# Performance work log

Measured on AMD Instinct MI355X. Metric: run time of the kernel, lower is better.

## Reference

```python
import jax, jax.numpy as jnp
import numpy as np

FP8_MAX = 448.0   # max finite value of float8_e4m3fn
GROUP = 128       # quant group size (both act cols and weight blocks)


def fp8_roundtrip(v):
    # Round-to-nearest onto the fp8 e4m3fn grid, back to f32.
    return v.astype(jnp.float8_e4m3fn).astype(jnp.float32)


def setup_inputs() -> dict:
    key = jax.random.key(0)
    k1, k2, k3 = jax.random.split(key, 3)
    M, H = 8192, 4096
    x = jax.random.normal(k1, (M, 2 * H), dtype=jnp.float32)
    # weight: rand -> fp8 grid (stored as f32 values lying exactly on fp8 grid)
    w_q = fp8_roundtrip(jax.random.uniform(k2, (H, H), dtype=jnp.float32))
    # per-(128,128)-block weight scales
    wscale = jax.random.uniform(k3, (H // GROUP, H // GROUP), dtype=jnp.float32)
    return {"x": x, "w_q": w_q, "wscale": wscale}


def reference(x, w_q, wscale):
    H = x.shape[-1] // 2
    # SiluAndMul: silu(gate) * up
    y = jax.nn.silu(x[:, :H]) * x[:, H:]            # [M, H]
    M = y.shape[0]
    # --- activation group quant, group shape (1, 128) ---
    g = y.reshape(M, H // GROUP, GROUP)
    amax = jnp.max(jnp.abs(g), axis=-1, keepdims=True)
    scale = jnp.maximum(amax, 1e-12) / FP8_MAX      # [M, H/128, 1]
    q = fp8_roundtrip(g / scale)                    # fp8-grid values
    y_dq = (q * scale).reshape(M, H)                # dequantized activation
    # --- weight block dequant, block shape (128, 128) ---
    nk, nn = H // GROUP, H // GROUP
    w_dq = (w_q.reshape(nk, GROUP, nn, GROUP) * wscale[:, None, :, None]).reshape(H, H)
    # block-fp8 linear: out[m, n] = sum_k y_dq[m, k] * w_dq[k, n]
    return y_dq @ w_dq
```

## Files before the change

kernel.cpp:

```cpp
#include <hip/hip_runtime.h>
#include <hip/hip_fp8.h>
#include <hip/hip_bf16.h>

#define MDIM 8192
#define HDIM 4096
#define NKT 64

typedef float f32x4 __attribute__((ext_vector_type(4)));
typedef short bf16x8 __attribute__((ext_vector_type(8)));
typedef unsigned short u16x4 __attribute__((ext_vector_type(4)));

__device__ inline void gload_lds16(const void* g, void* l) {
  __builtin_amdgcn_global_load_lds(
      (const __attribute__((address_space(1))) void*)g,
      (__attribute__((address_space(3))) void*)l, 16, 0, 0);
}

__device__ inline unsigned short f2bf(float f) {
  __hip_bfloat16 h = __float2bfloat16(f);
  return *reinterpret_cast<unsigned short*>(&h);
}

__global__ __launch_bounds__(256) void silu_quant_kernel(
    const float* __restrict__ x, unsigned short* __restrict__ yb) {
  const int m = blockIdx.x;
  const int t = threadIdx.x;
  const int g = t >> 3;
  const int i = t & 7;
  const float* xr = x + (size_t)m * (2 * HDIM);

  float v[16];
  float amax = 0.f;
#pragma unroll
  for (int j = 0; j < 4; ++j) {
    const int off = g * 128 + j * 32 + i * 4;
    f32x4 gate = *(const f32x4*)(xr + off);
    f32x4 up = *(const f32x4*)(xr + HDIM + off);
#pragma unroll
    for (int c = 0; c < 4; ++c) {
      float gg = gate[c];
      float s = gg / (1.f + expf(-gg));
      float val = s * up[c];
      v[j * 4 + c] = val;
      amax = fmaxf(amax, fabsf(val));
    }
  }
#pragma unroll
  for (int d = 1; d < 8; d <<= 1) amax = fmaxf(amax, __shfl_xor(amax, d, 64));
  const float scale = fmaxf(amax, 1e-12f) / 448.0f;

#pragma unroll
  for (int j = 0; j < 4; ++j) {
    u16x4 pk;
#pragma unroll
    for (int c = 0; c < 4; ++c) {
      __hip_fp8_e4m3 qv(v[j * 4 + c] / scale);
      pk[c] = f2bf((float)qv * scale);
    }
    *(u16x4*)(yb + (size_t)m * HDIM + g * 128 + j * 32 + i * 4) = pk;
  }
}

__global__ __launch_bounds__(256) void wconv_kernel(
    const float* __restrict__ w, const float* __restrict__ wsc,
    unsigned short* __restrict__ wt) {
  __shared__ unsigned short tile[64][66];
  const int t = threadIdx.x;
  const int n0 = (blockIdx.x & 63) * 64;
  const int k0 = (blockIdx.x >> 6) * 64;
  const float ws = wsc[(k0 >> 7) * 32 + (n0 >> 7)];
  {
    const int r = t >> 4;
    const int c4 = (t & 15) << 2;
#pragma unroll
    for (int j = 0; j < 4; ++j) {
      const int kr = r + j * 16;
      f32x4 vv = *(const f32x4*)(w + (size_t)(k0 + kr) * HDIM + n0 + c4);
#pragma unroll
      for (int c = 0; c < 4; ++c) tile[kr][c4 + c] = f2bf(vv[c] * ws);
    }
  }
  __syncthreads();
  {
    const int n = t >> 4;
    const int k4 = (t & 15) << 2;
#pragma unroll
    for (int j = 0; j < 4; ++j) {
      const int nn = n + j * 16;
      u16x4 pk;
#pragma unroll
      for (int c = 0; c < 4; ++c) pk[c] = tile[k4 + c][nn];
      *(u16x4*)(wt + (size_t)(n0 + nn) * HDIM + k0 + k4) = pk;
    }
  }
}

#define SCHED0 __builtin_amdgcn_sched_barrier(0)
#define SBAR do { SCHED0; __builtin_amdgcn_s_barrier(); SCHED0; } while (0)
#define VMW(n) asm volatile("s_waitcnt vmcnt(" #n ")" ::: "memory")
#define LGKM0 asm volatile("s_waitcnt lgkmcnt(0)" ::: "memory")
#define PRIO1 __builtin_amdgcn_s_setprio(1)
#define PRIO0 __builtin_amdgcn_s_setprio(0)

#define STAGE_UNIT(bi, kt, u) do {                                          \
    const __hip_bfloat16* gsrc;  unsigned char* ldst;                       \
    if ((u) == 0)      { gsrc = A + (size_t)(m0 + r0) * HDIM;       ldst = As[bi]; }          \
    else if ((u) == 1) { gsrc = B + (size_t)(n0 + r0) * HDIM;       ldst = Bs[bi]; }          \
    else if ((u) == 2) { gsrc = A + (size_t)(m0 + 128 + r0) * HDIM; ldst = As[bi] + 16384; }  \
    else               { gsrc = B + (size_t)(n0 + 128 + r0) * HDIM; ldst = Bs[bi] + 16384; }  \
    gsrc += (size_t)(kt) * 64 + cst * 8;                                    \
    gload_lds16(gsrc, ldst + t * 16);                                       \
    gload_lds16(gsrc + (size_t)64 * HDIM, ldst + 8192 + t * 16);            \
  } while (0)

#define RD_A(c, mh, dst) do { _Pragma("unroll") for (int mi = 0; mi < 4; ++mi) { \
    const int row = wm * 128 + (mh) * 64 + mi * 16 + lrow;                       \
    _Pragma("unroll") for (int kk = 0; kk < 2; ++kk)                             \
      dst[mi][kk] = *(const bf16x8*)(As[c] + row * 128 + (((kk * 4 + lhi) ^ rx) * 16)); \
  } } while (0)

#define RD_B(c, nh, dst) do { _Pragma("unroll") for (int ni = 0; ni < 2; ++ni) { \
    const int row = wn * 64 + (nh) * 32 + ni * 16 + lrow;                        \
    _Pragma("unroll") for (int kk = 0; kk < 2; ++kk)                             \
      dst[ni][kk] = *(const bf16x8*)(Bs[c] + row * 128 + (((kk * 4 + lhi) ^ rx) * 16)); \
  } } while (0)

#define MFMA16(AF, BF, MB, NB) do { _Pragma("unroll") for (int kk = 0; kk < 2; ++kk) \
    _Pragma("unroll") for (int mi = 0; mi < 4; ++mi)                                 \
      _Pragma("unroll") for (int ni = 0; ni < 2; ++ni)                               \
        acc[(MB) + mi][(NB) + ni] = __builtin_amdgcn_mfma_f32_16x16x32_bf16(         \
            AF[mi][kk], BF[ni][kk], acc[(MB) + mi][(NB) + ni], 0, 0, 0);             \
  } while (0)

#define ITER(j, SH123, SH0, VMSTMT) do {                                     \
    const int c_ = (j) & 1, n_ = c_ ^ 1;                                     \
                                                     \
    RD_A(c_, 0, afr0); RD_B(c_, 0, bfr0);                                    \
    if (SH123) STAGE_UNIT(n_, (j) + 1, 1);                                   \
    SCHED0;                                                                  \
    PRIO1; MFMA16(afr0, bfr0, 0, 0); PRIO0;                                  \
                                                     \
    RD_A(c_, 1, afr1);                                                       \
    if (SH123) STAGE_UNIT(n_, (j) + 1, 2);                                   \
    SCHED0;                                                                  \
    PRIO1; MFMA16(afr1, bfr0, 4, 0); PRIO0;                                  \
                                                     \
    RD_B(c_, 1, bfr1);                                                       \
    if (SH123) STAGE_UNIT(n_, (j) + 1, 3);                                   \
    SCHED0;                                                                  \
    PRIO1; MFMA16(afr1, bfr1, 4, 2); PRIO0;                                  \
    LGKM0; SBAR;                 \
                                                     \
    if (SH0) STAGE_UNIT(c_, (j) + 2, 0);                                     \
    SCHED0;                                                                  \
    PRIO1; MFMA16(afr0, bfr1, 0, 2); PRIO0;                                  \
    VMSTMT; SBAR;                                                            \
  } while (0)

__global__ __launch_bounds__(512, 1) void gemm_bf16_kernel(
    const __hip_bfloat16* __restrict__ A,
    const __hip_bfloat16* __restrict__ B,
    float* __restrict__ out) {
  __shared__ __align__(16) unsigned char As[2][32768];
  __shared__ __align__(16) unsigned char Bs[2][32768];

  const int bid = blockIdx.x;
  const int x = bid & 7, sub = bid >> 3;
  const int mtile = (x >> 1) * 8 + (sub & 7);
  const int ntile = (x & 1) * 8 + (sub >> 3);
  const int m0 = mtile * 256, n0 = ntile * 256;

  const int t = threadIdx.x;
  const int l = t & 63, wid = t >> 6;
  const int wm = wid >> 2, wn = wid & 3;
  const int lrow = l & 15, lhi = l >> 4;
  const int rx = lrow & 7;

  const int r0 = t >> 3;
  const int cst = (t & 7) ^ (r0 & 7);

  f32x4 acc[8][4];
#pragma unroll
  for (int a = 0; a < 8; ++a)
#pragma unroll
    for (int b = 0; b < 4; ++b) acc[a][b] = (f32x4){0.f, 0.f, 0.f, 0.f};
  bf16x8 afr0[4][2], afr1[4][2], bfr0[2][2], bfr1[2][2];

  STAGE_UNIT(0, 0, 0); STAGE_UNIT(0, 0, 1); STAGE_UNIT(0, 0, 2); STAGE_UNIT(0, 0, 3);
  STAGE_UNIT(1, 1, 0);
  VMW(2);
  SBAR;

  for (int j = 0; j <= NKT - 3; ++j) ITER(j, 1, 1, VMW(2));
  ITER(NKT - 2, 1, 0, VMW(0));
  ITER(NKT - 1, 0, 0, (void)0);

#pragma unroll
  for (int mi = 0; mi < 8; ++mi)
#pragma unroll
    for (int r = 0; r < 4; ++r) {
      const int grow = m0 + wm * 128 + mi * 16 + lhi * 4 + r;
      float* orow = out + (size_t)grow * HDIM + n0 + wn * 64 + lrow;
#pragma unroll
      for (int ni = 0; ni < 4; ++ni) orow[ni * 16] = acc[mi][ni][r];
    }
}

extern "C" void kernel_launch(void* const* d_in, const int* in_sizes, int n_in,
                              void* d_out, int out_size, void* d_ws, size_t ws_size,
                              hipStream_t stream) {
  const float* x = (const float*)d_in[0];
  const float* wq = (const float*)d_in[1];
  const float* wsc = (const float*)d_in[2];
  float* out = (float*)d_out;

  unsigned short* yb = (unsigned short*)d_ws;
  unsigned short* wt = yb + (size_t)MDIM * HDIM;

  silu_quant_kernel<<<MDIM, 256, 0, stream>>>(x, yb);
  wconv_kernel<<<(HDIM / 64) * (HDIM / 64), 256, 0, stream>>>(wq, wsc, wt);
  gemm_bf16_kernel<<<(MDIM / 256) * (HDIM / 256), 512, 0, stream>>>(
      (const __hip_bfloat16*)yb, (const __hip_bfloat16*)wt, out);
}
```

Before: 310.5 us.

## Simplify GEMM pipeline to single-tile prefetch with extra barriers per phase

Replaces the staggered prefetch schedule, where the A-low unit was loaded two k-tiles ahead and waits used vmcnt(2), with a plain double buffer. All four units of the next tile are issued in the first two phases, and the loop waits for vmcnt(0) at the end of each iteration. It adds a workgroup barrier around every MFMA phase, which lets the waves run in lockstep. The cost is less latency hiding, because each tile's loads must finish within one iteration, plus more barrier stalls.

```diff
diff --git a/kernel.cpp b/kernel.cpp
--- a/kernel.cpp
+++ b/kernel.cpp
@@ -97,7 +97,7 @@
 
 #define SCHED0 __builtin_amdgcn_sched_barrier(0)
 #define SBAR do { SCHED0; __builtin_amdgcn_s_barrier(); SCHED0; } while (0)
-#define VMW(n) asm volatile("s_waitcnt vmcnt(" #n ")" ::: "memory")
+#define VMW0 asm volatile("s_waitcnt vmcnt(0)" ::: "memory")
 #define LGKM0 asm volatile("s_waitcnt lgkmcnt(0)" ::: "memory")
 #define PRIO1 __builtin_amdgcn_s_setprio(1)
 #define PRIO0 __builtin_amdgcn_s_setprio(0)
@@ -132,29 +132,28 @@
             AF[mi][kk], BF[ni][kk], acc[(MB) + mi][(NB) + ni], 0, 0, 0);             \
   } while (0)
 
-#define ITER(j, SH123, SH0, VMSTMT) do {                                     \
+#define ITER(j, SH) do {                                                     \
     const int c_ = (j) & 1, n_ = c_ ^ 1;                                     \
-                                                     \
+                          \
     RD_A(c_, 0, afr0); RD_B(c_, 0, bfr0);                                    \
-    if (SH123) STAGE_UNIT(n_, (j) + 1, 1);                                   \
-    SCHED0;                                                                  \
+    if (SH) { STAGE_UNIT(n_, (j) + 1, 0); STAGE_UNIT(n_, (j) + 1, 1); }      \
+    SBAR; LGKM0; SCHED0;                                                     \
     PRIO1; MFMA16(afr0, bfr0, 0, 0); PRIO0;                                  \
-                                                     \
+    SBAR;                                                                    \
+                          \
     RD_A(c_, 1, afr1);                                                       \
-    if (SH123) STAGE_UNIT(n_, (j) + 1, 2);                                   \
-    SCHED0;                                                                  \
+    if (SH) { STAGE_UNIT(n_, (j) + 1, 2); STAGE_UNIT(n_, (j) + 1, 3); }      \
+    SBAR; LGKM0; SCHED0;                                                     \
     PRIO1; MFMA16(afr1, bfr0, 4, 0); PRIO0;                                  \
+    SBAR;                                                                    \
                                                      \
     RD_B(c_, 1, bfr1);                                                       \
-    if (SH123) STAGE_UNIT(n_, (j) + 1, 3);                                   \
-    SCHED0;                                                                  \
+    SBAR; LGKM0; SCHED0;                                                     \
     PRIO1; MFMA16(afr1, bfr1, 4, 2); PRIO0;                                  \
-    LGKM0; SBAR;                 \
-                                                     \
-    if (SH0) STAGE_UNIT(c_, (j) + 2, 0);                                     \
-    SCHED0;                                                                  \
+    SBAR;                                                                    \
+       \
     PRIO1; MFMA16(afr0, bfr1, 0, 2); PRIO0;                                  \
-    VMSTMT; SBAR;                                                            \
+    SCHED0; VMW0; SBAR;                                                      \
   } while (0)
 
 __global__ __launch_bounds__(512, 1) void gemm_bf16_kernel(
@@ -187,13 +186,11 @@
   bf16x8 afr0[4][2], afr1[4][2], bfr0[2][2], bfr1[2][2];
 
   STAGE_UNIT(0, 0, 0); STAGE_UNIT(0, 0, 1); STAGE_UNIT(0, 0, 2); STAGE_UNIT(0, 0, 3);
-  STAGE_UNIT(1, 1, 0);
-  VMW(2);
+  VMW0;
   SBAR;
 
-  for (int j = 0; j <= NKT - 3; ++j) ITER(j, 1, 1, VMW(2));
-  ITER(NKT - 2, 1, 0, VMW(0));
-  ITER(NKT - 1, 0, 0, (void)0);
+  for (int j = 0; j < NKT - 1; ++j) ITER(j, 1);
+  ITER(NKT - 1, 0);
 
 #pragma unroll
   for (int mi = 0; mi < 8; ++mi)
```

Result: slower. 330.3 us (+6.4%).

## Defer half of last MFMA block into next iteration with double-buffered fragments

Applied to the files above, without the earlier changes.

Splits the final MFMA group of each K-iteration by k-half. The second half is deferred into the start of the next iteration, so it overlaps that iteration's LDS fragment reads. Fragment registers are double-buffered (A/B sets alternating across iterations), and the loop is unrolled by two to keep register names static. This roughly doubles the fragment register footprint, which risks spills or pressure with 512 threads and launch bounds of one block.

```diff
diff --git a/kernel.cpp b/kernel.cpp
--- a/kernel.cpp
+++ b/kernel.cpp
@@ -132,29 +132,39 @@
             AF[mi][kk], BF[ni][kk], acc[(MB) + mi][(NB) + ni], 0, 0, 0);             \
   } while (0)
 
-#define ITER(j, SH123, SH0, VMSTMT) do {                                     \
-    const int c_ = (j) & 1, n_ = c_ ^ 1;                                     \
-                                                     \
-    RD_A(c_, 0, afr0); RD_B(c_, 0, bfr0);                                    \
-    if (SH123) STAGE_UNIT(n_, (j) + 1, 1);                                   \
-    SCHED0;                                                                  \
-    PRIO1; MFMA16(afr0, bfr0, 0, 0); PRIO0;                                  \
-                                                     \
-    RD_A(c_, 1, afr1);                                                       \
-    if (SH123) STAGE_UNIT(n_, (j) + 1, 2);                                   \
-    SCHED0;                                                                  \
-    PRIO1; MFMA16(afr1, bfr0, 4, 0); PRIO0;                                  \
-                                                     \
-    RD_B(c_, 1, bfr1);                                                       \
-    if (SH123) STAGE_UNIT(n_, (j) + 1, 3);                                   \
-    SCHED0;                                                                  \
-    PRIO1; MFMA16(afr1, bfr1, 4, 2); PRIO0;                                  \
-    LGKM0; SBAR;                 \
-                                                     \
-    if (SH0) STAGE_UNIT(c_, (j) + 2, 0);                                     \
-    SCHED0;                                                                  \
-    PRIO1; MFMA16(afr0, bfr1, 0, 2); PRIO0;                                  \
-    VMSTMT; SBAR;                                                            \
+#define MFMA8(AF, BF, MB, NB, KK) do {                                               \
+    _Pragma("unroll") for (int mi = 0; mi < 4; ++mi)                                 \
+      _Pragma("unroll") for (int ni = 0; ni < 2; ++ni)                               \
+        acc[(MB) + mi][(NB) + ni] = __builtin_amdgcn_mfma_f32_16x16x32_bf16(         \
+            AF[mi][KK], BF[ni][KK], acc[(MB) + mi][(NB) + ni], 0, 0, 0);             \
+  } while (0)
+
+#define ITER(j, AF0, AF1, BF0, BF1, PAF0, PBF1, DOP, SH123, SH4, VMSTMT) do { \
+    const int c_ = (j) & 1, n_ = c_ ^ 1;                                      \
+    \
+    RD_B(c_, 0, BF0); RD_A(c_, 0, AF0);                                       \
+    SCHED0;                                                                   \
+    if (DOP) { PRIO1; MFMA8(PAF0, PBF1, 0, 2, 1); PRIO0; }                    \
+    if (SH123) STAGE_UNIT(n_, (j) + 1, 1);                                    \
+    SCHED0;                                                                   \
+    PRIO1; MFMA16(AF0, BF0, 0, 0); PRIO0;                                     \
+                                                                      \
+    RD_A(c_, 1, AF1);                                                         \
+    if (SH123) STAGE_UNIT(n_, (j) + 1, 2);                                    \
+    SCHED0;                                                                   \
+    PRIO1; MFMA16(AF1, BF0, 4, 0); PRIO0;                                     \
+                                                                      \
+    RD_B(c_, 1, BF1);                                                         \
+    if (SH123) STAGE_UNIT(n_, (j) + 1, 3);                                    \
+    SCHED0;                                                                   \
+    PRIO1; MFMA16(AF1, BF1, 4, 2); PRIO0;                                     \
+    LGKM0; SBAR;                  \
+     \
+    if (SH4) STAGE_UNIT(c_, (j) + 2, 0);                                      \
+    SCHED0;                                                                   \
+    PRIO1; MFMA8(AF0, BF1, 0, 2, 0); PRIO0;                                   \
+    VMSTMT; SBAR;                                                             \
+                                     \
   } while (0)
 
 __global__ __launch_bounds__(512, 1) void gemm_bf16_kernel(
@@ -184,16 +194,23 @@
   for (int a = 0; a < 8; ++a)
 #pragma unroll
     for (int b = 0; b < 4; ++b) acc[a][b] = (f32x4){0.f, 0.f, 0.f, 0.f};
-  bf16x8 afr0[4][2], afr1[4][2], bfr0[2][2], bfr1[2][2];
+  bf16x8 afA0[4][2], afA1[4][2], bfA0[2][2], bfA1[2][2];
+  bf16x8 afB0[4][2], afB1[4][2], bfB0[2][2], bfB1[2][2];
 
   STAGE_UNIT(0, 0, 0); STAGE_UNIT(0, 0, 1); STAGE_UNIT(0, 0, 2); STAGE_UNIT(0, 0, 3);
   STAGE_UNIT(1, 1, 0);
   VMW(2);
   SBAR;
 
-  for (int j = 0; j <= NKT - 3; ++j) ITER(j, 1, 1, VMW(2));
-  ITER(NKT - 2, 1, 0, VMW(0));
-  ITER(NKT - 1, 0, 0, (void)0);
+  ITER(0, afA0, afA1, bfA0, bfA1, afB0, bfB1, 0, 1, 1, VMW(2));
+  ITER(1, afB0, afB1, bfB0, bfB1, afA0, bfA1, 1, 1, 1, VMW(2));
+  for (int j = 2; j <= NKT - 4; j += 2) {
+    ITER(j,     afA0, afA1, bfA0, bfA1, afB0, bfB1, 1, 1, 1, VMW(2));
+    ITER(j + 1, afB0, afB1, bfB0, bfB1, afA0, bfA1, 1, 1, 1, VMW(2));
+  }
+  ITER(NKT - 2, afA0, afA1, bfA0, bfA1, afB0, bfB1, 1, 1, 0, VMW(0));
+  ITER(NKT - 1, afB0, afB1, bfB0, bfB1, afA0, bfA1, 1, 0, 0, (void)0);
+  PRIO1; MFMA8(afB0, bfB1, 0, 2, 1); PRIO0;
 
 #pragma unroll
   for (int mi = 0; mi < 8; ++mi)
```

Result: slower. 328.6 us (+5.8%).
